# Kernel optimization log

Measured on AMD Instinct MI355X. Metric: run time of the kernel, lower is better.

## Reference

```python
import jax, jax.numpy as jnp
import numpy as np

SIGMA = 32.0        # Gaussian prior bandwidth (init sigma)
ADJ_RATIO = 0.2     # fraction of neighbors kept per row in feature adjacency
NEG_SLOPE = 0.01    # LeakyReLU slope
EPS = 1e-8


def setup_inputs() -> dict:
    key = jax.random.key(0)
    k0, k1, k2, k3 = jax.random.split(key, 4)
    N, D, L = 8192, 128, 2
    x = jax.random.normal(k0, (N, D), dtype=jnp.float32)
    importances = jax.random.uniform(k1, (N, 1), dtype=jnp.float32)
    W1 = jax.random.normal(k2, (L, D, D), dtype=jnp.float32) / np.float32(np.sqrt(D))
    W2 = jax.random.normal(k3, (L, D, D), dtype=jnp.float32) / np.float32(np.sqrt(D))
    return {"x": x, "importances": importances, "W1": W1, "W2": W2, "batch_size": N}


def _build_adj_prior(imp, eye):
    # Gaussian kernel on pairwise importance differences: [N,N]
    d = imp - imp.T
    A = jnp.exp(-(d * d) / SIGMA) + eye  # self loop
    return A / jnp.sum(A, axis=1, keepdims=True)  # row-normalize


def _build_adj_feature(x, eye, k):
    # cosine similarity, keep top adj_ratio*N entries per row, self loop, row-normalize
    xn = x / (jnp.linalg.norm(x, axis=1, keepdims=True) + EPS)
    S = xn @ xn.T  # [N,N]
    thr = jax.lax.top_k(S, k)[0][:, -1:]  # per-row k-th largest value
    A = jnp.where(S >= thr, S, jnp.zeros_like(S)) + eye
    return A / jnp.sum(A, axis=1, keepdims=True)


def reference(x, importances, W1, W2, batch_size):
    N = batch_size
    k = int(ADJ_RATIO * N)
    eye = jnp.eye(N, dtype=x.dtype)
    L = W1.shape[0]
    h = x
    for l in range(L):  # fixed small layer count
        h = x  # clone before layer (used in final residual)
        adj_prior = _build_adj_prior(importances, eye)
        adj_feat = _build_adj_feature(x, eye, k)
        # graph conv over both adjacencies: A @ (x @ W)
        x = jax.nn.leaky_relu(adj_prior @ (x @ W1[l]) + adj_feat @ (x @ W2[l]),
                              negative_slope=NEG_SLOPE)
    return x + h * importances
```

## Files before the change

### kernel.cpp

```cpp
#include <hip/hip_runtime.h>
#include <hip/hip_bf16.h>

typedef __bf16 bf16x8 __attribute__((ext_vector_type(8)));
typedef float f32x4 __attribute__((ext_vector_type(4)));
typedef unsigned short u16x2 __attribute__((ext_vector_type(2)));
typedef short s16x2 __attribute__((ext_vector_type(2)));
typedef unsigned u32x4 __attribute__((ext_vector_type(4)));
typedef __hip_bfloat16 bf16;

static constexpr int NN = 8192;
static constexpr int DD = 128;
static constexpr int KTOP = 1638;
static constexpr int KSLICE = 8;
static constexpr int KCH = NN / KSLICE;

__device__ __forceinline__ void gll16(const void* g, void* l) {
  __builtin_amdgcn_global_load_lds((const __attribute__((address_space(1))) void*)g,
                                   (__attribute__((address_space(3))) void*)l, 16, 0, 0);
}

__global__ void detect_dtype(const unsigned short* __restrict__ xin, int* __restrict__ flag) {
  __shared__ int cnt;
  if (threadIdx.x == 0) cnt = 0;
  __syncthreads();
  int c = 0;
  for (int i = threadIdx.x; i < 4096; i += 256) {
    int e = (xin[i] >> 7) & 0xFF;
    if (e >= 0x8A) ++c;
  }
  atomicAdd(&cnt, c);
  __syncthreads();
  if (threadIdx.x == 0) *flag = (cnt > 16) ? 1 : 0;
}

__global__ void prep(const void* __restrict__ imp_in,
                     const void* __restrict__ W1, const void* __restrict__ W2,
                     float* __restrict__ impf,
                     bf16* __restrict__ Wt1, bf16* __restrict__ Wt2,
                     const int* __restrict__ flag) {
  int isf32 = *flag;
  int b = blockIdx.x;
  if (b == 0) {
    for (int i = threadIdx.x; i < NN; i += 256)
      impf[i] = isf32 ? ((const float*)imp_in)[i] : __bfloat162float(((const bf16*)imp_in)[i]);
  } else {
    int w = b - 1;
    const void* srcv = (w < 2 ? W1 : W2);
    bf16* dst = (w < 2 ? Wt1 : Wt2) + (w & 1) * DD * DD;
    int off = (w & 1) * DD * DD;
    for (int f = threadIdx.x; f < DD * DD; f += 256) {
      int n = f >> 7, k = f & 127;
      float v = isf32 ? ((const float*)srcv)[off + k * DD + n]
                      : __bfloat162float(((const bf16*)srcv)[off + k * DD + n]);
      dst[n * DD + k] = __float2bfloat16(v);
    }
  }
}

__global__ void rownorm(const void* __restrict__ src, const int* __restrict__ flag, int raw,
                        bf16* __restrict__ xnb, bf16* __restrict__ xb) {
  int wave = threadIdx.x >> 6;
  int lane = threadIdx.x & 63;
  int row = blockIdx.x * 4 + wave;
  float vx, vy;
  if (raw && *flag == 0) {
    unsigned u = ((const unsigned*)src)[(long)row * 64 + lane];
    vx = __uint_as_float(u << 16);
    vy = __uint_as_float(u & 0xFFFF0000u);
  } else {
    float2 v = ((const float2*)src)[(long)row * 64 + lane];
    vx = v.x; vy = v.y;
  }
  float s = vx * vx + vy * vy;
  for (int off = 1; off < 64; off <<= 1) s += __shfl_xor(s, off);
  float inv = 1.0f / (sqrtf(s) + 1e-8f);
  int c = lane * 2;
  xb[(long)row * DD + c]      = __float2bfloat16(vx);
  xb[(long)row * DD + c + 1]  = __float2bfloat16(vy);
  xnb[(long)row * DD + c]     = __float2bfloat16(vx * inv);
  xnb[(long)row * DD + c + 1] = __float2bfloat16(vy * inv);
}

__launch_bounds__(256)
__global__ void prior_reduce(const float* __restrict__ impf, const bf16* __restrict__ Yt1,
                             float* __restrict__ Mt, float* __restrict__ Gt) {
  __shared__ float red[5][4];
  int c = blockIdx.x;
  int tid = threadIdx.x;
  float s[5] = {0.f, 0.f, 0.f, 0.f, 0.f};
  bool hasY = (c < 128);
  const bf16* col = Yt1 + (long)(hasY ? c : 0) * NN;
  for (int j = tid; j < NN; j += 256) {
    float d = impf[j];
    float a = __expf(d * d * (-1.0f / 32.0f));
    float p = hasY ? a * __bfloat162float(col[j]) : a;
    #pragma unroll
    for (int t = 0; t < 5; ++t) { s[t] += p; p *= d; }
  }
  #pragma unroll
  for (int t = 0; t < 5; ++t)
    for (int off = 1; off < 64; off <<= 1) s[t] += __shfl_xor(s[t], off);
  int wave = tid >> 6, lane = tid & 63;
  if (lane == 0)
    #pragma unroll
    for (int t = 0; t < 5; ++t) red[t][wave] = s[t];
  __syncthreads();
  if (tid == 0) {
    #pragma unroll
    for (int t = 0; t < 5; ++t) {
      float v = red[t][0] + red[t][1] + red[t][2] + red[t][3];
      if (hasY) Mt[t * 128 + c] = v; else Gt[t] = v;
    }
  }
}

__global__ void prior_vec(const float* __restrict__ impf, const float* __restrict__ Gt,
                          float* __restrict__ pvec) {
  int i = blockIdx.x * 256 + threadIdx.x;
  float d = impf[i];
  float a = __expf(d * d * (-1.0f / 32.0f));
  const float ct[5] = {1.0f, 1.0f / 16.0f, 1.0f / 512.0f, 1.0f / 24576.0f, 1.0f / 1572864.0f};
  float g[5];
  float p = a;
  #pragma unroll
  for (int t = 0; t < 5; ++t) { g[t] = ct[t] * p; p *= d; }
  float rs = 1.0f;
  #pragma unroll
  for (int t = 0; t < 5; ++t) rs += g[t] * Gt[t];
  float inv = 1.0f / rs;
  #pragma unroll
  for (int t = 0; t < 5; ++t) pvec[i * 8 + t] = g[t] * inv;
  pvec[i * 8 + 5] = inv;
}

__device__ __forceinline__ void gemm_core(const bf16* __restrict__ A, const bf16* __restrict__ Bt,
                                          long rowA0, long rowB0, int tid,
                                          bf16* __restrict__ Yt,
                                          bf16* __restrict__ RM, long rm_ld, bool relu) {
  __shared__ bf16 lA[128][136];
  __shared__ bf16 lB[64][136];
  for (int i = 0; i < 8; ++i) {
    int f = tid + i * 256;
    int r = f >> 4, kg = f & 15;
    *reinterpret_cast<uint4*>(&lA[r][kg * 8]) =
        *reinterpret_cast<const uint4*>(A + (rowA0 + r) * DD + kg * 8);
  }
  for (int i = 0; i < 4; ++i) {
    int f = tid + i * 256;
    int r = f >> 4, kg = f & 15;
    *reinterpret_cast<uint4*>(&lB[r][kg * 8]) =
        *reinterpret_cast<const uint4*>(Bt + (rowB0 + r) * DD + kg * 8);
  }
  __syncthreads();
  int wave = tid >> 6, lane = tid & 63;
  int wm = (wave >> 1) * 64;
  int wn = (wave & 1) * 32;
  int quad = lane >> 4, l16 = lane & 15;
  f32x4 acc[4][2];
  #pragma unroll
  for (int mi = 0; mi < 4; ++mi)
    #pragma unroll
    for (int ni = 0; ni < 2; ++ni) acc[mi][ni] = {0.f, 0.f, 0.f, 0.f};
  #pragma unroll
  for (int ks = 0; ks < 4; ++ks) {
    int kb = ks * 32 + quad * 8;
    bf16x8 af[4], bfr[2];
    #pragma unroll
    for (int mi = 0; mi < 4; ++mi)
      af[mi] = *reinterpret_cast<const bf16x8*>(&lA[wm + mi * 16 + l16][kb]);
    #pragma unroll
    for (int ni = 0; ni < 2; ++ni)
      bfr[ni] = *reinterpret_cast<const bf16x8*>(&lB[wn + ni * 16 + l16][kb]);
    #pragma unroll
    for (int mi = 0; mi < 4; ++mi)
      #pragma unroll
      for (int ni = 0; ni < 2; ++ni)
        acc[mi][ni] = __builtin_amdgcn_mfma_f32_16x16x32_bf16(af[mi], bfr[ni], acc[mi][ni], 0, 0, 0);
  }
  if (Yt) {
    #pragma unroll
    for (int mi = 0; mi < 4; ++mi)
      #pragma unroll
      for (int ni = 0; ni < 2; ++ni) {
        long rowb = rowA0 + wm + mi * 16 + quad * 4;
        long col = rowB0 + wn + ni * 16 + l16;
        bf16 t4[4];
        #pragma unroll
        for (int r = 0; r < 4; ++r) t4[r] = __float2bfloat16(acc[mi][ni][r]);
        *reinterpret_cast<ushort4*>(Yt + col * (long)NN + rowb) =
            *reinterpret_cast<const ushort4*>(t4);
      }
  }
  __syncthreads();
  bf16 (*cs)[72] = reinterpret_cast<bf16(*)[72]>(&lA[0][0]);
  #pragma unroll
  for (int mi = 0; mi < 4; ++mi)
    #pragma unroll
    for (int ni = 0; ni < 2; ++ni)
      #pragma unroll
      for (int r = 0; r < 4; ++r) {
        float vv = acc[mi][ni][r];
        if (relu) vv = vv > 0.f ? vv : 0.f;
        cs[wm + mi * 16 + quad * 4 + r][wn + ni * 16 + l16] = __float2bfloat16(vv);
      }
  __syncthreads();
  #pragma unroll
  for (int i = 0; i < 4; ++i) {
    int f = tid + i * 256;
    int r = f >> 3, sg = f & 7;
    *reinterpret_cast<uint4*>(RM + (rowA0 + r) * rm_ld + rowB0 + sg * 8) =
        *reinterpret_cast<const uint4*>(&cs[r][sg * 8]);
  }
}

__launch_bounds__(256)
__global__ void gemm_s(const bf16* __restrict__ Xn, bf16* __restrict__ S) {
  gemm_core(Xn, Xn, (long)blockIdx.y * 128, (long)blockIdx.x * 64, threadIdx.x,
            nullptr, S, NN, true);
}

__launch_bounds__(256)
__global__ void gemm_y_dual(const bf16* __restrict__ xb,
                            const bf16* __restrict__ Wt1, const bf16* __restrict__ Wt2,
                            bf16* __restrict__ Yt1, bf16* __restrict__ Yt2,
                            bf16* __restrict__ Yr1, bf16* __restrict__ Yr2) {
  int sel = blockIdx.x >> 1;
  int bx = blockIdx.x & 1;
  gemm_core(xb, sel ? Wt2 : Wt1, (long)blockIdx.y * 128, (long)bx * 64, threadIdx.x,
            sel ? Yt2 : Yt1, sel ? Yr2 : Yr1, DD, false);
}

__launch_bounds__(256)
__global__ void topk_thresh(const bf16* __restrict__ S, unsigned short* __restrict__ kthr,
                            float* __restrict__ invRsF) {
  __shared__ unsigned hist[4][1088];
  int wave = threadIdx.x >> 6, lane = threadIdx.x & 63;
  long row = (long)blockIdx.x * 4 + wave;
  unsigned* h = hist[wave];
  #pragma unroll
  for (int j = 0; j < 17; ++j) h[lane + j * 64] = 0;
  __syncthreads();

  const uint4* rp = reinterpret_cast<const uint4*>(S + row * NN) + lane;
  unsigned hs = 0;
  #pragma unroll
  for (int t = 0; t < 16; ++t) {
    uint4 v = rp[t * 64];
    unsigned a4[4] = {v.x, v.y, v.z, v.w};
    #pragma unroll
    for (int e = 0; e < 4; ++e) {
      unsigned u = a4[e];
      hs |= u;
      s16x2 d = __builtin_bit_cast(s16x2, u) - __builtin_bit_cast(s16x2, 0x3BFF3BFFu);
      d = __builtin_elementwise_max(d, (s16x2)0);
      d = __builtin_elementwise_min(d, (s16x2)1024);
      unsigned bins = __builtin_bit_cast(unsigned, d);
      unsigned blo = bins & 0xFFFFu, bhi = bins >> 16;
      if (blo) atomicAdd(&h[blo], 1u);
      if (bhi) atomicAdd(&h[bhi], 1u);
    }
  }
  __syncthreads();

  unsigned c[17], sfx[17];
  #pragma unroll
  for (int j = 0; j < 17; ++j) c[j] = h[lane * 17 + j];
  unsigned run = 0;
  #pragma unroll
  for (int j = 16; j >= 0; --j) { run += c[j]; sfx[j] = run; }
  unsigned incl = sfx[0];
  #pragma unroll
  for (int off = 1; off < 64; off <<= 1) {
    unsigned t = __shfl_down(incl, off);
    incl += (lane + off < 64) ? t : 0u;
  }
  unsigned above = incl - sfx[0];
  int cand = -1;
  #pragma unroll
  for (int j = 16; j >= 0; --j) {
    int b = lane * 17 + j;
    if (cand < 0 && b >= 1 && above + sfx[j] >= (unsigned)KTOP) cand = b;
  }
  int best = cand;
  #pragma unroll
  for (int off = 1; off < 64; off <<= 1) {
    int t = __shfl_xor(best, off);
    best = t > best ? t : best;
  }
  int thrbin = best >= 1 ? best : 1;
  unsigned thr = 0x3BFFu + (unsigned)thrbin;

  float fs = 0.f;
  #pragma unroll
  for (int j = 0; j < 17; ++j) {
    int b = lane * 17 + j;
    float val = __uint_as_float((0x3BFFu + (unsigned)b) << 16);
    fs += (b >= thrbin) ? (float)c[j] * val : 0.f;
  }
  if (__ballot(hs & 0x40004000u)) {
    float v1024 = __uint_as_float(0x3FFF0000u);
    #pragma unroll 1
    for (int t = 0; t < 16; ++t) {
      uint4 v = rp[t * 64];
      unsigned a4[4] = {v.x, v.y, v.z, v.w};
      for (int e = 0; e < 4; ++e) {
        unsigned lo = a4[e] & 0xFFFFu, hi = a4[e] >> 16;
        if (lo >= 0x4000u && lo < 0x8000u) fs += __uint_as_float(lo << 16) - v1024;
        if (hi >= 0x4000u && hi < 0x8000u) fs += __uint_as_float(hi << 16) - v1024;
      }
    }
  }
  #pragma unroll
  for (int off = 1; off < 64; off <<= 1) fs += __shfl_xor(fs, off);
  if (lane == 0) {
    invRsF[row] = 1.0f / (fs + 1.0f);
    kthr[row] = (unsigned short)thr;
  }
}

__launch_bounds__(256)
__global__ void fused_av_partial(const bf16* __restrict__ S, const bf16* __restrict__ Yt2,
                                 const unsigned short* __restrict__ kthr,
                                 float* __restrict__ Pacc) {
  __shared__ bf16 lS[2][128][64];
  __shared__ bf16 lY[2][128][64];
  int tid = threadIdx.x;
  int wave = tid >> 6, lane = tid & 63;
  long row0 = (long)blockIdx.x * 128;
  long kbase = (long)blockIdx.y * KCH;
  int quad = lane >> 4, l16 = lane & 15;
  int wm = (wave >> 1) * 64;
  int wn = (wave & 1) * 64;
  int swz = (l16 & 7) << 4;

  int sj = lane >> 3, sseg = lane & 7;
  long swb = (long)((sseg ^ sj) << 4);
  const char* gS[4];
  const char* gY[4];
  #pragma unroll
  for (int j = 0; j < 4; ++j) {
    long srow = row0 + (long)(wave * 4 + j) * 8 + sj;
    gS[j] = (const char*)S + (srow * NN + kbase) * 2 + swb;
    long ycol = (long)(wave * 4 + j) * 8 + sj;
    gY[j] = (const char*)Yt2 + (ycol * (long)NN + kbase) * 2 + swb;
  }
  unsigned pp[4];
  #pragma unroll
  for (int mi = 0; mi < 4; ++mi) {
    unsigned p = kthr[row0 + wm + mi * 16 + l16];
    pp[mi] = (p << 16) | p;
  }
  f32x4 acc[4][4];
  #pragma unroll
  for (int mi = 0; mi < 4; ++mi)
    #pragma unroll
    for (int ni = 0; ni < 4; ++ni) acc[mi][ni] = {0.f, 0.f, 0.f, 0.f};

  constexpr int NT = KCH / 64;
  {
    char* lsb = (char*)&lS[0][0][0];
    char* lyb = (char*)&lY[0][0][0];
    #pragma unroll
    for (int j = 0; j < 4; ++j) { gll16(gS[j], lsb + (wave * 4 + j) * 1024); gS[j] += 128; }
    #pragma unroll
    for (int j = 0; j < 4; ++j) { gll16(gY[j], lyb + (wave * 4 + j) * 1024); gY[j] += 128; }
  }
  #pragma unroll 1
  for (int t = 0; t < NT; ++t) {
    int cur = t & 1;
    if (t + 1 < NT) {
      char* lsb = (char*)&lS[cur ^ 1][0][0];
      char* lyb = (char*)&lY[cur ^ 1][0][0];
      #pragma unroll
      for (int j = 0; j < 4; ++j) { gll16(gS[j], lsb + (wave * 4 + j) * 1024); gS[j] += 128; }
      #pragma unroll
      for (int j = 0; j < 4; ++j) { gll16(gY[j], lyb + (wave * 4 + j) * 1024); gY[j] += 128; }
      asm volatile("s_waitcnt vmcnt(8)" ::: "memory");
    } else {
      asm volatile("s_waitcnt vmcnt(0)" ::: "memory");
    }
    __builtin_amdgcn_s_barrier();
    const char* lsb = (const char*)&lS[cur][0][0];
    const char* lyb = (const char*)&lY[cur][0][0];
    #pragma unroll
    for (int ks = 0; ks < 2; ++ks) {
      int cb = ks * 64 + quad * 16;
      int cbs = cb ^ swz;
      bf16x8 av[4], bv[4];
      #pragma unroll
      for (int mi = 0; mi < 4; ++mi) {
        int r = wm + mi * 16 + l16;
        u32x4 uu = *reinterpret_cast<const u32x4*>(lsb + r * 128 + cbs);
        #pragma unroll
        for (int e = 0; e < 4; ++e) {
          unsigned tb = uu[e] | 0x80008000u;
          u16x2 d = __builtin_bit_cast(u16x2, tb) - __builtin_bit_cast(u16x2, pp[mi]);
          s16x2 msk = __builtin_bit_cast(s16x2, d) >> 15;
          uu[e] &= __builtin_bit_cast(unsigned, msk);
        }
        av[mi] = __builtin_bit_cast(bf16x8, uu);
      }
      #pragma unroll
      for (int ni = 0; ni < 4; ++ni) {
        int c = wn + ni * 16 + l16;
        bv[ni] = *reinterpret_cast<const bf16x8*>(lyb + c * 128 + cbs);
      }
      #pragma unroll
      for (int mi = 0; mi < 4; ++mi)
        #pragma unroll
        for (int ni = 0; ni < 4; ++ni)
          acc[mi][ni] = __builtin_amdgcn_mfma_f32_16x16x32_bf16(av[mi], bv[ni], acc[mi][ni], 0, 0, 0);
    }
    __builtin_amdgcn_s_barrier();
  }
  float* out = Pacc + (long)blockIdx.y * NN * DD;
  #pragma unroll
  for (int mi = 0; mi < 4; ++mi)
    #pragma unroll
    for (int ni = 0; ni < 4; ++ni)
      #pragma unroll
      for (int r = 0; r < 4; ++r) {
        long row = row0 + wm + mi * 16 + quad * 4 + r;
        int col = wn + ni * 16 + l16;
        out[row * DD + col] = acc[mi][ni][r];
      }
}

__global__ void epilogue(const float* __restrict__ Pacc, const bf16* __restrict__ Yr1,
                         const bf16* __restrict__ Yr2, const float* __restrict__ pvec,
                         const float* __restrict__ Mt, const float* __restrict__ invRsF,
                         float* __restrict__ Xout, const float* __restrict__ hres,
                         const float* __restrict__ impf, float* __restrict__ outf) {
  int i = blockIdx.x * 256 + threadIdx.x;
  int row = i >> 7, col = i & 127;
  float acc = 0.f;
  #pragma unroll
  for (int s = 0; s < KSLICE; ++s) acc += Pacc[((long)s * NN + row) * DD + col];
  const float* pv = pvec + row * 8;
  float y1 = __bfloat162float(Yr1[i]);
  float y2 = __bfloat162float(Yr2[i]);
  float prior = pv[5] * y1 + pv[0] * Mt[col] + pv[1] * Mt[128 + col] + pv[2] * Mt[256 + col]
              + pv[3] * Mt[384 + col] + pv[4] * Mt[512 + col];
  float v = prior + invRsF[row] * (acc + y2);
  v = v > 0.f ? v : 0.01f * v;
  if (outf) outf[i] = v + hres[i] * impf[row];
  else      Xout[i] = v;
}


extern "C" void kernel_launch(void* const* d_in, const int* in_sizes, int n_in,
                              void* d_out, int out_size, void* d_ws, size_t ws_size,
                              hipStream_t stream) {
  const void* x_in   = d_in[0];
  const void* imp_in = d_in[1];
  const void* W1 = d_in[2];
  const void* W2 = d_in[3];
  float* out = (float*)d_out;

  char* ws = (char*)d_ws;
  size_t o = 0;
  auto alloc = [&](size_t bytes) { void* p = ws + o; o += (bytes + 511) & ~511ull; return p; };
  bf16*  Af   = (bf16*)alloc((size_t)NN * NN * 2);
  float* Pacc = (float*)alloc((size_t)KSLICE * NN * DD * 4);
  float* xf1  = (float*)alloc((size_t)NN * DD * 4);
  bf16*  xnb  = (bf16*)alloc((size_t)NN * DD * 2);
  bf16*  xb   = (bf16*)alloc((size_t)NN * DD * 2);
  bf16*  Yt1  = (bf16*)alloc((size_t)NN * DD * 2);
  bf16*  Yt2  = (bf16*)alloc((size_t)NN * DD * 2);
  bf16*  Yr1  = (bf16*)alloc((size_t)NN * DD * 2);
  bf16*  Yr2  = (bf16*)alloc((size_t)NN * DD * 2);
  bf16*  Wt1  = (bf16*)alloc((size_t)2 * DD * DD * 2);
  bf16*  Wt2  = (bf16*)alloc((size_t)2 * DD * DD * 2);
  float* impf = (float*)alloc((size_t)NN * 4);
  float* pvec = (float*)alloc((size_t)NN * 8 * 4);
  float* Mt   = (float*)alloc((size_t)5 * 128 * 4);
  float* Gt   = (float*)alloc((size_t)8 * 4);
  float* invRsF = (float*)alloc((size_t)NN * 4);
  unsigned short* kthr = (unsigned short*)alloc((size_t)NN * 2);
  int*   dflag  = (int*)alloc(64);
  (void)ws_size; (void)n_in; (void)in_sizes; (void)out_size;

  detect_dtype<<<1, 256, 0, stream>>>((const unsigned short*)x_in, dflag);
  prep<<<5, 256, 0, stream>>>(imp_in, W1, W2, impf, Wt1, Wt2, dflag);

  for (int l = 0; l < 2; ++l) {
    rownorm<<<NN / 4, 256, 0, stream>>>(l ? (const void*)xf1 : x_in, dflag, l ? 0 : 1, xnb, xb);
    gemm_y_dual<<<dim3(4, 64), 256, 0, stream>>>(xb, Wt1 + l * DD * DD, Wt2 + l * DD * DD,
                                                 Yt1, Yt2, Yr1, Yr2);
    prior_reduce<<<129, 256, 0, stream>>>(impf, Yt1, Mt, Gt);
    prior_vec<<<NN / 256, 256, 0, stream>>>(impf, Gt, pvec);
    gemm_s<<<dim3(NN / 64, NN / 128), 256, 0, stream>>>(xnb, Af);
    topk_thresh<<<NN / 4, 256, 0, stream>>>(Af, kthr, invRsF);
    fused_av_partial<<<dim3(NN / 128, KSLICE), 256, 0, stream>>>(Af, Yt2, kthr, Pacc);
    if (l == 0)
      epilogue<<<NN * DD / 256, 256, 0, stream>>>(Pacc, Yr1, Yr2, pvec, Mt, invRsF,
                                                  xf1, nullptr, nullptr, nullptr);
    else
      epilogue<<<NN * DD / 256, 256, 0, stream>>>(Pacc, Yr1, Yr2, pvec, Mt, invRsF,
                                                  nullptr, xf1, impf, out);
  }
}
```

Before: 357.5 us.

## Exploit symmetry of similarity matrix and fold prior vector into epilogue

The S = Xn·Xnᵀ GEMM now computes only upper-triangle 128x128 tiles and writes each tile both directly and transposed, roughly halving the MFMA work and input loads for this N×N product. Separately, the prior_vec kernel is removed and its per-row Gaussian-moment coefficients are recomputed inside the epilogue, saving one launch and the pvec round trip. The transposed stores are scattered 8-byte writes, and half the launched blocks exit immediately. The epilogue now does redundant per-element exp and divide work in place of that launch.

```diff
diff --git a/kernel.cpp b/kernel.cpp
--- a/kernel.cpp
+++ b/kernel.cpp
@@ -114,29 +114,10 @@
   }
 }
 
-__global__ void prior_vec(const float* __restrict__ impf, const float* __restrict__ Gt,
-                          float* __restrict__ pvec) {
-  int i = blockIdx.x * 256 + threadIdx.x;
-  float d = impf[i];
-  float a = __expf(d * d * (-1.0f / 32.0f));
-  const float ct[5] = {1.0f, 1.0f / 16.0f, 1.0f / 512.0f, 1.0f / 24576.0f, 1.0f / 1572864.0f};
-  float g[5];
-  float p = a;
-  #pragma unroll
-  for (int t = 0; t < 5; ++t) { g[t] = ct[t] * p; p *= d; }
-  float rs = 1.0f;
-  #pragma unroll
-  for (int t = 0; t < 5; ++t) rs += g[t] * Gt[t];
-  float inv = 1.0f / rs;
-  #pragma unroll
-  for (int t = 0; t < 5; ++t) pvec[i * 8 + t] = g[t] * inv;
-  pvec[i * 8 + 5] = inv;
-}
-
 __device__ __forceinline__ void gemm_core(const bf16* __restrict__ A, const bf16* __restrict__ Bt,
                                           long rowA0, long rowB0, int tid,
                                           bf16* __restrict__ Yt,
-                                          bf16* __restrict__ RM, long rm_ld, bool relu) {
+                                          bf16* __restrict__ RM, long rm_ld) {
   __shared__ bf16 lA[128][136];
   __shared__ bf16 lB[64][136];
   for (int i = 0; i < 8; ++i) {
@@ -198,11 +179,8 @@
     #pragma unroll
     for (int ni = 0; ni < 2; ++ni)
       #pragma unroll
-      for (int r = 0; r < 4; ++r) {
-        float vv = acc[mi][ni][r];
-        if (relu) vv = vv > 0.f ? vv : 0.f;
-        cs[wm + mi * 16 + quad * 4 + r][wn + ni * 16 + l16] = __float2bfloat16(vv);
-      }
+      for (int r = 0; r < 4; ++r)
+        cs[wm + mi * 16 + quad * 4 + r][wn + ni * 16 + l16] = __float2bfloat16(acc[mi][ni][r]);
   __syncthreads();
   #pragma unroll
   for (int i = 0; i < 4; ++i) {
@@ -214,9 +192,88 @@
 }
 
 __launch_bounds__(256)
-__global__ void gemm_s(const bf16* __restrict__ Xn, bf16* __restrict__ S) {
-  gemm_core(Xn, Xn, (long)blockIdx.y * 128, (long)blockIdx.x * 64, threadIdx.x,
-            nullptr, S, NN, true);
+__global__ void gemm_s_sym(const bf16* __restrict__ Xn, bf16* __restrict__ S) {
+  int bi = blockIdx.y, bj = blockIdx.x;
+  if (bj < bi) return;
+  __shared__ bf16 lA[128][136];
+  __shared__ bf16 lB[128][136];
+  int tid = threadIdx.x;
+  long rowA0 = (long)bi * 128, rowB0 = (long)bj * 128;
+  for (int i = 0; i < 8; ++i) {
+    int f = tid + i * 256;
+    int r = f >> 4, kg = f & 15;
+    *reinterpret_cast<uint4*>(&lA[r][kg * 8]) =
+        *reinterpret_cast<const uint4*>(Xn + (rowA0 + r) * DD + kg * 8);
+    *reinterpret_cast<uint4*>(&lB[r][kg * 8]) =
+        *reinterpret_cast<const uint4*>(Xn + (rowB0 + r) * DD + kg * 8);
+  }
+  __syncthreads();
+  int wave = tid >> 6, lane = tid & 63;
+  int wm = (wave >> 1) * 64;
+  int wn = (wave & 1) * 64;
+  int quad = lane >> 4, l16 = lane & 15;
+  f32x4 acc[4][4];
+  #pragma unroll
+  for (int mi = 0; mi < 4; ++mi)
+    #pragma unroll
+    for (int ni = 0; ni < 4; ++ni) acc[mi][ni] = {0.f, 0.f, 0.f, 0.f};
+  #pragma unroll
+  for (int ks = 0; ks < 4; ++ks) {
+    int kb = ks * 32 + quad * 8;
+    bf16x8 af[4], bfr[4];
+    #pragma unroll
+    for (int mi = 0; mi < 4; ++mi)
+      af[mi] = *reinterpret_cast<const bf16x8*>(&lA[wm + mi * 16 + l16][kb]);
+    #pragma unroll
+    for (int ni = 0; ni < 4; ++ni)
+      bfr[ni] = *reinterpret_cast<const bf16x8*>(&lB[wn + ni * 16 + l16][kb]);
+    #pragma unroll
+    for (int mi = 0; mi < 4; ++mi)
+      #pragma unroll
+      for (int ni = 0; ni < 4; ++ni)
+        acc[mi][ni] = __builtin_amdgcn_mfma_f32_16x16x32_bf16(af[mi], bfr[ni], acc[mi][ni], 0, 0, 0);
+  }
+  unsigned short q4[4][4][4];
+  #pragma unroll
+  for (int mi = 0; mi < 4; ++mi)
+    #pragma unroll
+    for (int ni = 0; ni < 4; ++ni)
+      #pragma unroll
+      for (int r = 0; r < 4; ++r) {
+        float vv = acc[mi][ni][r];
+        vv = vv > 0.f ? vv : 0.f;
+        bf16 b = __float2bfloat16(vv);
+        q4[mi][ni][r] = *reinterpret_cast<unsigned short*>(&b);
+      }
+  if (bi != bj) {
+    #pragma unroll
+    for (int mi = 0; mi < 4; ++mi)
+      #pragma unroll
+      for (int ni = 0; ni < 4; ++ni) {
+        long rowb = rowA0 + wm + mi * 16 + quad * 4;
+        long col = rowB0 + wn + ni * 16 + l16;
+        *reinterpret_cast<ushort4*>(S + col * (long)NN + rowb) =
+            *reinterpret_cast<const ushort4*>(q4[mi][ni]);
+      }
+  }
+  __syncthreads();
+  bf16 (*cs)[136] = reinterpret_cast<bf16(*)[136]>(&lA[0][0]);
+  #pragma unroll
+  for (int mi = 0; mi < 4; ++mi)
+    #pragma unroll
+    for (int ni = 0; ni < 4; ++ni)
+      #pragma unroll
+      for (int r = 0; r < 4; ++r)
+        *reinterpret_cast<unsigned short*>(&cs[wm + mi * 16 + quad * 4 + r][wn + ni * 16 + l16]) =
+            q4[mi][ni][r];
+  __syncthreads();
+  #pragma unroll
+  for (int i = 0; i < 8; ++i) {
+    int f = tid + i * 256;
+    int r = f >> 4, sg = f & 15;
+    *reinterpret_cast<uint4*>(S + (rowA0 + r) * NN + rowB0 + sg * 8) =
+        *reinterpret_cast<const uint4*>(&cs[r][sg * 8]);
+  }
 }
 
 __launch_bounds__(256)
@@ -227,7 +284,7 @@
   int sel = blockIdx.x >> 1;
   int bx = blockIdx.x & 1;
   gemm_core(xb, sel ? Wt2 : Wt1, (long)blockIdx.y * 128, (long)bx * 64, threadIdx.x,
-            sel ? Yt2 : Yt1, sel ? Yr2 : Yr1, DD, false);
+            sel ? Yt2 : Yt1, sel ? Yr2 : Yr1, DD);
 }
 
 __launch_bounds__(256)
@@ -427,19 +484,33 @@
 }
 
 __global__ void epilogue(const float* __restrict__ Pacc, const bf16* __restrict__ Yr1,
-                         const bf16* __restrict__ Yr2, const float* __restrict__ pvec,
+                         const bf16* __restrict__ Yr2, const float* __restrict__ Gt,
                          const float* __restrict__ Mt, const float* __restrict__ invRsF,
+                         const float* __restrict__ impf,
                          float* __restrict__ Xout, const float* __restrict__ hres,
-                         const float* __restrict__ impf, float* __restrict__ outf) {
+                         float* __restrict__ outf) {
   int i = blockIdx.x * 256 + threadIdx.x;
   int row = i >> 7, col = i & 127;
   float acc = 0.f;
   #pragma unroll
   for (int s = 0; s < KSLICE; ++s) acc += Pacc[((long)s * NN + row) * DD + col];
-  const float* pv = pvec + row * 8;
+  float d = impf[row];
+  float a = __expf(d * d * (-1.0f / 32.0f));
+  const float ct[5] = {1.0f, 1.0f / 16.0f, 1.0f / 512.0f, 1.0f / 24576.0f, 1.0f / 1572864.0f};
+  float g[5];
+  float p = a;
+  #pragma unroll
+  for (int t = 0; t < 5; ++t) { g[t] = ct[t] * p; p *= d; }
+  float rs = 1.0f;
+  #pragma unroll
+  for (int t = 0; t < 5; ++t) rs += g[t] * Gt[t];
+  float inv = 1.0f / rs;
+  float pv[5];
+  #pragma unroll
+  for (int t = 0; t < 5; ++t) pv[t] = g[t] * inv;
   float y1 = __bfloat162float(Yr1[i]);
   float y2 = __bfloat162float(Yr2[i]);
-  float prior = pv[5] * y1 + pv[0] * Mt[col] + pv[1] * Mt[128 + col] + pv[2] * Mt[256 + col]
+  float prior = inv * y1 + pv[0] * Mt[col] + pv[1] * Mt[128 + col] + pv[2] * Mt[256 + col]
               + pv[3] * Mt[384 + col] + pv[4] * Mt[512 + col];
   float v = prior + invRsF[row] * (acc + y2);
   v = v > 0.f ? v : 0.01f * v;
@@ -472,7 +543,6 @@
   bf16*  Wt1  = (bf16*)alloc((size_t)2 * DD * DD * 2);
   bf16*  Wt2  = (bf16*)alloc((size_t)2 * DD * DD * 2);
   float* impf = (float*)alloc((size_t)NN * 4);
-  float* pvec = (float*)alloc((size_t)NN * 8 * 4);
   float* Mt   = (float*)alloc((size_t)5 * 128 * 4);
   float* Gt   = (float*)alloc((size_t)8 * 4);
   float* invRsF = (float*)alloc((size_t)NN * 4);
@@ -488,15 +558,14 @@
     gemm_y_dual<<<dim3(4, 64), 256, 0, stream>>>(xb, Wt1 + l * DD * DD, Wt2 + l * DD * DD,
                                                  Yt1, Yt2, Yr1, Yr2);
     prior_reduce<<<129, 256, 0, stream>>>(impf, Yt1, Mt, Gt);
-    prior_vec<<<NN / 256, 256, 0, stream>>>(impf, Gt, pvec);
-    gemm_s<<<dim3(NN / 64, NN / 128), 256, 0, stream>>>(xnb, Af);
+    gemm_s_sym<<<dim3(64, 64), 256, 0, stream>>>(xnb, Af);
     topk_thresh<<<NN / 4, 256, 0, stream>>>(Af, kthr, invRsF);
     fused_av_partial<<<dim3(NN / 128, KSLICE), 256, 0, stream>>>(Af, Yt2, kthr, Pacc);
     if (l == 0)
-      epilogue<<<NN * DD / 256, 256, 0, stream>>>(Pacc, Yr1, Yr2, pvec, Mt, invRsF,
-                                                  xf1, nullptr, nullptr, nullptr);
+      epilogue<<<NN * DD / 256, 256, 0, stream>>>(Pacc, Yr1, Yr2, Gt, Mt, invRsF, impf,
+                                                  xf1, nullptr, nullptr);
     else
-      epilogue<<<NN * DD / 256, 256, 0, stream>>>(Pacc, Yr1, Yr2, pvec, Mt, invRsF,
-                                                  nullptr, xf1, impf, out);
-  }
-}
+      epilogue<<<NN * DD / 256, 256, 0, stream>>>(Pacc, Yr1, Yr2, Gt, Mt, invRsF, impf,
+                                                  nullptr, xf1, out);
+  }
+}
```

New measurement: 366.8 us. +2.6%, slower.
